# Optimization experiments

Measured on AMD Instinct MI355X. Metric: run time of the kernel, lower is better.

Reference implementation:

```python
import jax, jax.numpy as jnp
import numpy as np

NUM_CLASSES = 6
CE_W, DICE_W, FT_W = 0.4, 0.4, 0.2
FT_ALPHA, FT_BETA, FT_GAMMA = 0.7, 0.3, 1.33


def setup_inputs() -> dict:
    key = jax.random.key(0)
    k1, k2 = jax.random.split(key)
    logits = jax.random.normal(k1, (16, NUM_CLASSES, 512, 512), dtype=jnp.float32)
    targets = jax.random.randint(k2, (16, 512, 512), 0, NUM_CLASSES, dtype=jnp.int64)
    return {"logits": logits, "targets": targets}


def reference(logits, targets):
    B, C, H, W = logits.shape
    # ---- shared: log-softmax / softmax over class dim (computed once) ----
    logp = jax.nn.log_softmax(logits, axis=1)          # (B,C,H,W)
    probs = jnp.exp(logp)

    # ---- Cross entropy (mean over all pixels) ----
    lp_t = jnp.take_along_axis(logp, targets[:, None, :, :], axis=1)[:, 0]  # (B,H,W)
    ce = -lp_t.mean()

    # ---- per-class sufficient statistics (no full one-hot kept around) ----
    oh = (targets[:, None, :, :] == jnp.arange(C, dtype=targets.dtype)[None, :, None, None])
    oh = oh.astype(probs.dtype)                         # (B,C,H,W)
    TP = jnp.sum(probs * oh, axis=(2, 3))               # (B,C)
    p_sum = jnp.sum(probs, axis=(2, 3))                 # (B,C)
    t_sum = jnp.sum(oh, axis=(2, 3))                    # (B,C)

    # ---- Dice ----
    dice = (2.0 * TP + 1e-8) / (p_sum + t_sum + 1e-8)   # (B,C)
    dice_loss = jnp.mean(1.0 - dice)                    # mean over B and C

    # ---- Focal Tversky ----
    FP = p_sum - TP
    FN = t_sum - TP
    tversky = (TP + 1e-6) / (TP + FT_ALPHA * FN + FT_BETA * FP + 1e-6)
    ft_loss = jnp.mean((1.0 - tversky) ** FT_GAMMA)

    return CE_W * ce + DICE_W * dice_loss + FT_W * ft_loss
```

## Files before the change

### kernel.cpp

```cpp
#include <hip/hip_runtime.h>

#define BATCH 16
#define NCLS 6
#define HW 262144
#define BLOCKS_PER_B 64
#define THREADS 256
#define ITERS 4

#define NACC 19

__global__ __launch_bounds__(THREADS) void loss_main(
    const float* __restrict__ logits,
    const int*   __restrict__ targets,
    float*       __restrict__ ws) {
    const int b   = blockIdx.y;
    const int tid = threadIdx.x;

    float acc[NACC];
    #pragma unroll
    for (int i = 0; i < NACC; ++i) acc[i] = 0.f;

    const float* lbase = logits + (size_t)b * NCLS * HW;
    const int4*  tbase = (const int4*)(targets + (size_t)b * HW);

    for (int k = 0; k < ITERS; ++k) {
        const int p4 = k * (BLOCKS_PER_B * THREADS) + blockIdx.x * THREADS + tid;

        float L[4][NCLS];
        #pragma unroll
        for (int c = 0; c < NCLS; ++c) {
            float4 v = ((const float4*)(lbase + (size_t)c * HW))[p4];
            L[0][c] = v.x; L[1][c] = v.y; L[2][c] = v.z; L[3][c] = v.w;
        }
        const int4 tv4 = tbase[p4];
        const int tgt[4] = {tv4.x, tv4.y, tv4.z, tv4.w};

        #pragma unroll
        for (int j = 0; j < 4; ++j) {
            float m = L[j][0];
            #pragma unroll
            for (int c = 1; c < NCLS; ++c) m = fmaxf(m, L[j][c]);

            float e[NCLS];
            float s = 0.f;
            #pragma unroll
            for (int c = 0; c < NCLS; ++c) { e[c] = __expf(L[j][c] - m); s += e[c]; }
            const float inv = 1.0f / s;
            const float lse = m + __logf(s);

            #pragma unroll
            for (int c = 0; c < NCLS; ++c) {
                const float pr = e[c] * inv;
                acc[6 + c] += pr;
                const bool is_t = (tgt[j] == c);
                acc[c]      += is_t ? pr  : 0.f;
                acc[12 + c] += is_t ? 1.f : 0.f;
                acc[18]     += is_t ? (lse - L[j][c]) : 0.f;
            }
        }
    }

    #pragma unroll
    for (int i = 0; i < NACC; ++i) {
        float v = acc[i];
        v += __shfl_down(v, 32);
        v += __shfl_down(v, 16);
        v += __shfl_down(v, 8);
        v += __shfl_down(v, 4);
        v += __shfl_down(v, 2);
        v += __shfl_down(v, 1);
        acc[i] = v;
    }

    __shared__ float sacc[NACC];
    if (tid < NACC) sacc[tid] = 0.f;
    __syncthreads();
    if ((tid & 63) == 0) {
        #pragma unroll
        for (int i = 0; i < NACC; ++i) atomicAdd(&sacc[i], acc[i]);
    }
    __syncthreads();
    if (tid < NACC) atomicAdd(&ws[b * NACC + tid], sacc[tid]);
}

__global__ __launch_bounds__(128) void loss_finalize(
    const float* __restrict__ ws, float* __restrict__ out) {
    __shared__ float sd[128], sf[128], sc[128];
    const int i = threadIdx.x;
    float dice = 0.f, ft = 0.f, ce = 0.f;
    if (i < BATCH * NCLS) {
        const int b = i / NCLS, c = i % NCLS;
        const float* w = ws + b * NACC;
        const float TP = w[c], PS = w[6 + c], TS = w[12 + c];
        const float d = (2.f * TP + 1e-8f) / (PS + TS + 1e-8f);
        dice = 1.f - d;
        const float FP = PS - TP;
        const float FN = TS - TP;
        const float tv = (TP + 1e-6f) / (TP + 0.7f * FN + 0.3f * FP + 1e-6f);
        ft = powf(fmaxf(1.f - tv, 0.f), 1.33f);
    }
    if (i < BATCH) ce = ws[i * NACC + 18];
    sd[i] = dice; sf[i] = ft; sc[i] = ce;
    __syncthreads();
    for (int s = 64; s > 0; s >>= 1) {
        if (i < s) { sd[i] += sd[i + s]; sf[i] += sf[i + s]; sc[i] += sc[i + s]; }
        __syncthreads();
    }
    if (i == 0) {
        const float ce_mean   = sc[0] / (float)((size_t)BATCH * HW);
        const float dice_loss = sd[0] / (float)(BATCH * NCLS);
        const float ft_loss   = sf[0] / (float)(BATCH * NCLS);
        out[0] = 0.4f * ce_mean + 0.4f * dice_loss + 0.2f * ft_loss;
    }
}

extern "C" void kernel_launch(void* const* d_in, const int* in_sizes, int n_in,
                              void* d_out, int out_size, void* d_ws, size_t ws_size,
                              hipStream_t stream) {
    const float* logits  = (const float*)d_in[0];
    const int*   targets = (const int*)d_in[1];
    float*       ws      = (float*)d_ws;

    hipMemsetAsync(ws, 0, BATCH * NACC * sizeof(float), stream);

    loss_main<<<dim3(BLOCKS_PER_B, BATCH), THREADS, 0, stream>>>(logits, targets, ws);
    loss_finalize<<<1, 128, 0, stream>>>(ws, (float*)d_out);
}
```

Baseline: 167.7 us.

## Replace global atomics and memset with per-block partials reduced in finalize

Each block now writes its partial sums to a dedicated workspace slot instead of atomically adding into a zeroed buffer, so the memset launch goes away. The finalize kernel sums the 64 partials per batch. Target counts use wave ballot/popcount instead of per-lane float accumulation, the reciprocal uses the hardware rcp, and the target logit is selected once per pixel. This cuts ALU and register work and removes one stream operation, at the cost of a slightly longer finalize loop.

```diff
diff --git a/kernel.cpp b/kernel.cpp
--- a/kernel.cpp
+++ b/kernel.cpp
@@ -14,17 +14,21 @@
     const int*   __restrict__ targets,
     float*       __restrict__ ws) {
     const int b   = blockIdx.y;
+    const int bx  = blockIdx.x;
     const int tid = threadIdx.x;
 
-    float acc[NACC];
+    float facc[13];
     #pragma unroll
-    for (int i = 0; i < NACC; ++i) acc[i] = 0.f;
+    for (int i = 0; i < 13; ++i) facc[i] = 0.f;
+    int tcnt[NCLS];
+    #pragma unroll
+    for (int c = 0; c < NCLS; ++c) tcnt[c] = 0;
 
     const float* lbase = logits + (size_t)b * NCLS * HW;
     const int4*  tbase = (const int4*)(targets + (size_t)b * HW);
 
     for (int k = 0; k < ITERS; ++k) {
-        const int p4 = k * (BLOCKS_PER_B * THREADS) + blockIdx.x * THREADS + tid;
+        const int p4 = k * (BLOCKS_PER_B * THREADS) + bx * THREADS + tid;
 
         float L[4][NCLS];
         #pragma unroll
@@ -45,31 +49,33 @@
             float s = 0.f;
             #pragma unroll
             for (int c = 0; c < NCLS; ++c) { e[c] = __expf(L[j][c] - m); s += e[c]; }
-            const float inv = 1.0f / s;
+            const float inv = __builtin_amdgcn_rcpf(s);
             const float lse = m + __logf(s);
 
+            float Lt = 0.f;
             #pragma unroll
             for (int c = 0; c < NCLS; ++c) {
                 const float pr = e[c] * inv;
-                acc[6 + c] += pr;
+                facc[6 + c] += pr;
                 const bool is_t = (tgt[j] == c);
-                acc[c]      += is_t ? pr  : 0.f;
-                acc[12 + c] += is_t ? 1.f : 0.f;
-                acc[18]     += is_t ? (lse - L[j][c]) : 0.f;
+                facc[c] += is_t ? pr : 0.f;
+                Lt = is_t ? L[j][c] : Lt;
+                tcnt[c] += (int)__popcll(__ballot(is_t));
             }
+            facc[12] += lse - Lt;
         }
     }
 
     #pragma unroll
-    for (int i = 0; i < NACC; ++i) {
-        float v = acc[i];
+    for (int i = 0; i < 13; ++i) {
+        float v = facc[i];
         v += __shfl_down(v, 32);
         v += __shfl_down(v, 16);
         v += __shfl_down(v, 8);
         v += __shfl_down(v, 4);
         v += __shfl_down(v, 2);
         v += __shfl_down(v, 1);
-        acc[i] = v;
+        facc[i] = v;
     }
 
     __shared__ float sacc[NACC];
@@ -77,10 +83,16 @@
     __syncthreads();
     if ((tid & 63) == 0) {
         #pragma unroll
-        for (int i = 0; i < NACC; ++i) atomicAdd(&sacc[i], acc[i]);
+        for (int i = 0; i < 6; ++i) atomicAdd(&sacc[i], facc[i]);
+        #pragma unroll
+        for (int i = 0; i < 6; ++i) atomicAdd(&sacc[6 + i], facc[6 + i]);
+        #pragma unroll
+        for (int c = 0; c < NCLS; ++c) atomicAdd(&sacc[12 + c], (float)tcnt[c]);
+        atomicAdd(&sacc[18], facc[12]);
     }
     __syncthreads();
-    if (tid < NACC) atomicAdd(&ws[b * NACC + tid], sacc[tid]);
+    if (tid < NACC)
+        ws[(tid * BATCH + b) * BLOCKS_PER_B + bx] = sacc[tid];
 }
 
 __global__ __launch_bounds__(128) void loss_finalize(
@@ -90,8 +102,13 @@
     float dice = 0.f, ft = 0.f, ce = 0.f;
     if (i < BATCH * NCLS) {
         const int b = i / NCLS, c = i % NCLS;
-        const float* w = ws + b * NACC;
-        const float TP = w[c], PS = w[6 + c], TS = w[12 + c];
+        float TP = 0.f, PS = 0.f, TS = 0.f;
+        #pragma unroll 8
+        for (int k = 0; k < BLOCKS_PER_B; ++k) {
+            TP += ws[((c)      * BATCH + b) * BLOCKS_PER_B + k];
+            PS += ws[((6 + c)  * BATCH + b) * BLOCKS_PER_B + k];
+            TS += ws[((12 + c) * BATCH + b) * BLOCKS_PER_B + k];
+        }
         const float d = (2.f * TP + 1e-8f) / (PS + TS + 1e-8f);
         dice = 1.f - d;
         const float FP = PS - TP;
@@ -99,7 +116,11 @@
         const float tv = (TP + 1e-6f) / (TP + 0.7f * FN + 0.3f * FP + 1e-6f);
         ft = powf(fmaxf(1.f - tv, 0.f), 1.33f);
     }
-    if (i < BATCH) ce = ws[i * NACC + 18];
+    if (i < BATCH) {
+        #pragma unroll 8
+        for (int k = 0; k < BLOCKS_PER_B; ++k)
+            ce += ws[(18 * BATCH + i) * BLOCKS_PER_B + k];
+    }
     sd[i] = dice; sf[i] = ft; sc[i] = ce;
     __syncthreads();
     for (int s = 64; s > 0; s >>= 1) {
@@ -121,8 +142,6 @@
     const int*   targets = (const int*)d_in[1];
     float*       ws      = (float*)d_ws;
 
-    hipMemsetAsync(ws, 0, BATCH * NACC * sizeof(float), stream);
-
     loss_main<<<dim3(BLOCKS_PER_B, BATCH), THREADS, 0, stream>>>(logits, targets, ws);
     loss_finalize<<<1, 128, 0, stream>>>(ws, (float*)d_out);
 }
```

Measured after the change: 168.0 us. Within noise of the previous version (+0.2%).
